# Performance work log

Measured on AMD Instinct MI355X. Metric: run time of the kernel, lower is better.

## Reference

```python
import jax, jax.numpy as jnp
import numpy as np

LOG2PI = float(np.log(2.0 * np.pi))


def _diag_gauss_logprob(x, mean, var):
    # clamp variance like torch's clamp_min(1e-10)
    var = jnp.maximum(var, 1e-10)
    return -0.5 * jnp.sum(jnp.log(var) + LOG2PI + (x - mean) ** 2 / var, axis=-1)


def setup_inputs() -> dict:
    key = jax.random.key(0)
    k1, k2, k3, k4, k5 = jax.random.split(key, 5)
    B, T, D = 256, 1024, 256
    y = jax.random.normal(k1, (B, T, D), dtype=jnp.float32)
    # strictly increasing time grid per dim (broadcast 2D form [T, D])
    dt = jax.random.uniform(k2, (T, D), dtype=jnp.float32, minval=1e-3, maxval=1e-2)
    ts_batch = jnp.cumsum(dt, axis=0)
    # learned params around their torch inits (mu=0.0, logk=logs=-0.7)
    mu = 0.0 + 0.05 * jax.random.normal(k3, (D,), dtype=jnp.float32)
    log_kappa = -0.7 + 0.05 * jax.random.normal(k4, (D,), dtype=jnp.float32)
    log_sigma = -0.7 + 0.05 * jax.random.normal(k5, (D,), dtype=jnp.float32)
    return {"y": y, "ts_batch": ts_batch, "mu": mu,
            "log_kappa": log_kappa, "log_sigma": log_sigma}


def reference(y, ts_batch, mu, log_kappa, log_sigma):
    # y: [B, T, D]; ts_batch: [T, D] (or [B, T, D]); params: [D]
    kappa = jax.nn.softplus(log_kappa) + 1e-6
    sigma = jax.nn.softplus(log_sigma) + 1e-6
    if ts_batch.ndim == 2:
        ts = ts_batch[None, :, :]  # broadcast over batch
    else:
        ts = ts_batch

    # stationary initial distribution: N(mu, sigma^2 / (2 kappa))
    var0 = sigma ** 2 / (2.0 * kappa)
    lp0 = _diag_gauss_logprob(y[:, 0, :], mu, var0)  # [B]

    # exact OU transition densities for all steps at once
    dt = jnp.maximum(ts[:, 1:, :] - ts[:, :-1, :], 1e-6)  # [*, T-1, D]
    Ad = jnp.exp(-kappa * dt)
    mean = mu + Ad * (y[:, :-1, :] - mu)                  # [B, T-1, D]
    q = sigma ** 2 * (1.0 - jnp.exp(-2.0 * kappa * dt)) / (2.0 * kappa)
    lp_trans = jnp.sum(_diag_gauss_logprob(y[:, 1:, :], mean, q), axis=1)  # [B]
    return lp0 + lp_trans
```

## Files before the change

kernel.cpp:

```cpp
#include <hip/hip_runtime.h>

#define LOG2PI 1.8378770664093453f

__global__ __launch_bounds__(256) void ou_lp_kernel(
    const float* __restrict__ y,
    const float* __restrict__ ts,
    const float* __restrict__ mu,
    const float* __restrict__ lk,
    const float* __restrict__ ls,
    float* __restrict__ out,
    int B, int T, int D)
{
    const int b    = blockIdx.y;
    const int widx = threadIdx.x >> 6;
    const int lane = threadIdx.x & 63;
    const int d4   = lane * 4;
    const int NW   = gridDim.x * 4;
    const int gw   = blockIdx.x * 4 + widx;
    const int NT   = T - 1;
    const int lo   = 1 + (NT * gw) / NW;
    const int hi   = 1 + (NT * (gw + 1)) / NW;

    const float4 muv = *(const float4*)(mu + d4);
    const float4 lkv = *(const float4*)(lk + d4);
    const float4 lsv = *(const float4*)(ls + d4);

    float mur[4]   = {muv.x, muv.y, muv.z, muv.w};
    float lkr[4]   = {lkv.x, lkv.y, lkv.z, lkv.w};
    float lsr[4]   = {lsv.x, lsv.y, lsv.z, lsv.w};
    float kap[4], s2[4], inv2k[4];
    #pragma unroll
    for (int j = 0; j < 4; ++j) {
        float xk = lkr[j];
        float kappa = fmaxf(xk, 0.0f) + log1pf(__expf(-fabsf(xk)));
        kappa += 1e-6f;
        float xs = lsr[j];
        float sigma = fmaxf(xs, 0.0f) + log1pf(__expf(-fabsf(xs)));
        sigma += 1e-6f;
        kap[j]   = kappa;
        s2[j]    = sigma * sigma;
        inv2k[j] = 0.5f / kappa;
    }

    const size_t ybase = (size_t)b * T * D;
    float ypc[4], tsp[4], acc[4];
    {
        const float4 y0 = *(const float4*)(y  + ybase + (size_t)(lo - 1) * D + d4);
        const float4 t0 = *(const float4*)(ts + (size_t)(lo - 1) * D + d4);
        ypc[0] = y0.x - mur[0]; ypc[1] = y0.y - mur[1];
        ypc[2] = y0.z - mur[2]; ypc[3] = y0.w - mur[3];
        tsp[0] = t0.x; tsp[1] = t0.y; tsp[2] = t0.z; tsp[3] = t0.w;
    }
    acc[0] = acc[1] = acc[2] = acc[3] = 0.0f;

    if (gw == 0) {
        #pragma unroll
        for (int j = 0; j < 4; ++j) {
            float var0 = fmaxf(s2[j] * inv2k[j], 1e-10f);
            float yc   = ypc[j];
            acc[j] += __logf(var0) + LOG2PI + __fdividef(yc * yc, var0);
        }
    }

    for (int t = lo; t < hi; ++t) {
        const float4 yt = *(const float4*)(y  + ybase + (size_t)t * D + d4);
        const float4 tt = *(const float4*)(ts + (size_t)t * D + d4);
        float ytr[4] = {yt.x, yt.y, yt.z, yt.w};
        float ttr[4] = {tt.x, tt.y, tt.z, tt.w};
        #pragma unroll
        for (int j = 0; j < 4; ++j) {
            float dt = fmaxf(ttr[j] - tsp[j], 1e-6f);
            float e  = __expf(-kap[j] * dt);
            float q  = fmaxf(s2[j] * (1.0f - e * e) * inv2k[j], 1e-10f);
            float yc = ytr[j] - mur[j];
            float r  = yc - e * ypc[j];
            acc[j] += __logf(q) + LOG2PI + __fdividef(r * r, q);
            ypc[j] = yc;
            tsp[j] = ttr[j];
        }
    }

    float s = (acc[0] + acc[1]) + (acc[2] + acc[3]);
    #pragma unroll
    for (int off = 32; off > 0; off >>= 1)
        s += __shfl_down(s, off);

    __shared__ float wsum[4];
    if (lane == 0) wsum[widx] = s;
    __syncthreads();
    if (threadIdx.x == 0) {
        float tot = (wsum[0] + wsum[1]) + (wsum[2] + wsum[3]);
        atomicAdd(out + b, -0.5f * tot);
    }
}

extern "C" void kernel_launch(void* const* d_in, const int* in_sizes, int n_in,
                              void* d_out, int out_size, void* d_ws, size_t ws_size,
                              hipStream_t stream) {
    const float* y  = (const float*)d_in[0];
    const float* ts = (const float*)d_in[1];
    const float* mu = (const float*)d_in[2];
    const float* lk = (const float*)d_in[3];
    const float* ls = (const float*)d_in[4];
    float* out = (float*)d_out;

    const int D = in_sizes[2];
    const int T = in_sizes[1] / D;
    const int B = in_sizes[0] / (T * D);

    hipMemsetAsync(d_out, 0, (size_t)out_size * sizeof(float), stream);

    dim3 grid(4, B);
    dim3 block(256);
    ou_lp_kernel<<<grid, block, 0, stream>>>(y, ts, mu, lk, ls, out, B, T, D);
}
```

Measured before the change: 400.4 us.

## Precompute batch-invariant OU transition terms once, then run a streaming quadratic-form kernel

Adds a precompute kernel that evaluates the time-grid and parameter terms once over [T, D], since none of them depend on the batch. It stores the decay factor and the inverse transition variance to workspace and sums the log-variance constants into one scalar. The main kernel then only streams y with a few FMAs per element, instead of doing an exp, a log and a divide per element in every batch. It also doubles the grid width, adds a one-step register prefetch, and adds a second launch, an extra memset and an atomic accumulation of the constant.

```diff
diff --git a/kernel.cpp b/kernel.cpp
--- a/kernel.cpp
+++ b/kernel.cpp
@@ -2,12 +2,66 @@
 
 #define LOG2PI 1.8378770664093453f
 
-__global__ __launch_bounds__(256) void ou_lp_kernel(
+
+__device__ __forceinline__ float block_reduce_add(float v, float* lds) {
+    #pragma unroll
+    for (int off = 32; off > 0; off >>= 1)
+        v += __shfl_down(v, off);
+    const int widx = threadIdx.x >> 6;
+    const int lane = threadIdx.x & 63;
+    if (lane == 0) lds[widx] = v;
+    __syncthreads();
+    float tot = 0.0f;
+    if (threadIdx.x == 0) {
+        const int nw = blockDim.x >> 6;
+        for (int i = 0; i < nw; ++i) tot += lds[i];
+    }
+    return tot;
+}
+
+__global__ void ou_precompute_kernel(
+    const float* __restrict__ ts, const float* __restrict__ lk,
+    const float* __restrict__ ls,
+    float* __restrict__ C, float* __restrict__ invvar0,
+    float* __restrict__ Ad, float* __restrict__ invq,
+    int T, int D)
+{
+    const int t = blockIdx.x;
+    const int d = threadIdx.x;
+
+    float xk = lk[d];
+    float kappa = fmaxf(xk, 0.0f) + log1pf(expf(-fabsf(xk))) + 1e-6f;
+    float xs = ls[d];
+    float sg = fmaxf(xs, 0.0f) + log1pf(expf(-fabsf(xs))) + 1e-6f;
+    float s2 = sg * sg;
+    float inv2k = 0.5f / kappa;
+
+    float val;
+    if (t == 0) {
+        float var0 = fmaxf(s2 * inv2k, 1e-10f);
+        invvar0[d] = 1.0f / var0;
+        val = logf(var0) + LOG2PI;
+    } else {
+        float dt = fmaxf(ts[t * D + d] - ts[(t - 1) * D + d], 1e-6f);
+        float e  = expf(-kappa * dt);
+        float q  = fmaxf(s2 * (1.0f - e * e) * inv2k, 1e-10f);
+        Ad[t * D + d]   = e;
+        invq[t * D + d] = 1.0f / q;
+        val = logf(q) + LOG2PI;
+    }
+
+    __shared__ float lds[8];
+    float tot = block_reduce_add(val, lds);
+    if (threadIdx.x == 0) atomicAdd(C, tot);
+}
+
+__global__ __launch_bounds__(256, 8) void ou_quad_kernel(
     const float* __restrict__ y,
-    const float* __restrict__ ts,
     const float* __restrict__ mu,
-    const float* __restrict__ lk,
-    const float* __restrict__ ls,
+    const float* __restrict__ C,
+    const float* __restrict__ invvar0,
+    const float* __restrict__ Ad,
+    const float* __restrict__ invq,
     float* __restrict__ out,
     int B, int T, int D)
 {
@@ -22,62 +76,51 @@
     const int hi   = 1 + (NT * (gw + 1)) / NW;
 
     const float4 muv = *(const float4*)(mu + d4);
-    const float4 lkv = *(const float4*)(lk + d4);
-    const float4 lsv = *(const float4*)(ls + d4);
-
-    float mur[4]   = {muv.x, muv.y, muv.z, muv.w};
-    float lkr[4]   = {lkv.x, lkv.y, lkv.z, lkv.w};
-    float lsr[4]   = {lsv.x, lsv.y, lsv.z, lsv.w};
-    float kap[4], s2[4], inv2k[4];
-    #pragma unroll
-    for (int j = 0; j < 4; ++j) {
-        float xk = lkr[j];
-        float kappa = fmaxf(xk, 0.0f) + log1pf(__expf(-fabsf(xk)));
-        kappa += 1e-6f;
-        float xs = lsr[j];
-        float sigma = fmaxf(xs, 0.0f) + log1pf(__expf(-fabsf(xs)));
-        sigma += 1e-6f;
-        kap[j]   = kappa;
-        s2[j]    = sigma * sigma;
-        inv2k[j] = 0.5f / kappa;
-    }
+    float mur[4] = {muv.x, muv.y, muv.z, muv.w};
 
     const size_t ybase = (size_t)b * T * D;
-    float ypc[4], tsp[4], acc[4];
+    float ypc[4], acc[4];
     {
-        const float4 y0 = *(const float4*)(y  + ybase + (size_t)(lo - 1) * D + d4);
-        const float4 t0 = *(const float4*)(ts + (size_t)(lo - 1) * D + d4);
+        const float4 y0 = *(const float4*)(y + ybase + (size_t)(lo - 1) * D + d4);
         ypc[0] = y0.x - mur[0]; ypc[1] = y0.y - mur[1];
         ypc[2] = y0.z - mur[2]; ypc[3] = y0.w - mur[3];
-        tsp[0] = t0.x; tsp[1] = t0.y; tsp[2] = t0.z; tsp[3] = t0.w;
     }
     acc[0] = acc[1] = acc[2] = acc[3] = 0.0f;
 
     if (gw == 0) {
+        const float4 iv = *(const float4*)(invvar0 + d4);
+        float ivr[4] = {iv.x, iv.y, iv.z, iv.w};
+        #pragma unroll
+        for (int j = 0; j < 4; ++j) acc[j] += ypc[j] * ypc[j] * ivr[j];
+    }
+
+    const float* yp = y   + ybase + (size_t)lo * D + d4;
+    const float* ap = Ad  + (size_t)lo * D + d4;
+    const float* qp = invq + (size_t)lo * D + d4;
+
+    float4 ycur = *(const float4*)yp;
+    float4 acur = *(const float4*)ap;
+    float4 qcur = *(const float4*)qp;
+    for (int t = lo; t < hi; ++t) {
+        float4 ynxt, anxt, qnxt;
+        if (t + 1 < hi) {
+            ynxt = *(const float4*)(yp + D);
+            anxt = *(const float4*)(ap + D);
+            qnxt = *(const float4*)(qp + D);
+        }
+        yp += D; ap += D; qp += D;
+
+        float ytr[4] = {ycur.x, ycur.y, ycur.z, ycur.w};
+        float adr[4] = {acur.x, acur.y, acur.z, acur.w};
+        float iqr[4] = {qcur.x, qcur.y, qcur.z, qcur.w};
         #pragma unroll
         for (int j = 0; j < 4; ++j) {
-            float var0 = fmaxf(s2[j] * inv2k[j], 1e-10f);
-            float yc   = ypc[j];
-            acc[j] += __logf(var0) + LOG2PI + __fdividef(yc * yc, var0);
+            float yc = ytr[j] - mur[j];
+            float r  = fmaf(-adr[j], ypc[j], yc);
+            acc[j]   = fmaf(r * r, iqr[j], acc[j]);
+            ypc[j]   = yc;
         }
-    }
-
-    for (int t = lo; t < hi; ++t) {
-        const float4 yt = *(const float4*)(y  + ybase + (size_t)t * D + d4);
-        const float4 tt = *(const float4*)(ts + (size_t)t * D + d4);
-        float ytr[4] = {yt.x, yt.y, yt.z, yt.w};
-        float ttr[4] = {tt.x, tt.y, tt.z, tt.w};
-        #pragma unroll
-        for (int j = 0; j < 4; ++j) {
-            float dt = fmaxf(ttr[j] - tsp[j], 1e-6f);
-            float e  = __expf(-kap[j] * dt);
-            float q  = fmaxf(s2[j] * (1.0f - e * e) * inv2k[j], 1e-10f);
-            float yc = ytr[j] - mur[j];
-            float r  = yc - e * ypc[j];
-            acc[j] += __logf(q) + LOG2PI + __fdividef(r * r, q);
-            ypc[j] = yc;
-            tsp[j] = ttr[j];
-        }
+        ycur = ynxt; acur = anxt; qcur = qnxt;
     }
 
     float s = (acc[0] + acc[1]) + (acc[2] + acc[3]);
@@ -90,6 +133,7 @@
     __syncthreads();
     if (threadIdx.x == 0) {
         float tot = (wsum[0] + wsum[1]) + (wsum[2] + wsum[3]);
+        if (blockIdx.x == 0) tot += C[0];
         atomicAdd(out + b, -0.5f * tot);
     }
 }
@@ -108,9 +152,19 @@
     const int T = in_sizes[1] / D;
     const int B = in_sizes[0] / (T * D);
 
+    char* ws = (char*)d_ws;
+    float* C       = (float*)(ws);
+    float* invvar0 = (float*)(ws + 256);
+    float* Ad      = (float*)(ws + 4096);
+    float* invq    = (float*)(ws + 4096 + (size_t)T * D * sizeof(float));
+
     hipMemsetAsync(d_out, 0, (size_t)out_size * sizeof(float), stream);
+    hipMemsetAsync(C, 0, sizeof(float), stream);
 
-    dim3 grid(4, B);
-    dim3 block(256);
-    ou_lp_kernel<<<grid, block, 0, stream>>>(y, ts, mu, lk, ls, out, B, T, D);
+    ou_precompute_kernel<<<dim3(T), dim3(D), 0, stream>>>(
+        ts, lk, ls, C, invvar0, Ad, invq, T, D);
+
+    dim3 grid(8, B);
+    ou_quad_kernel<<<grid, dim3(256), 0, stream>>>(
+        y, mu, C, invvar0, Ad, invq, out, B, T, D);
 }
```

Measured after the change: 386.8 us. 3.4% less time.

## Process two batches per thread to share time-dependent transcendentals and prefetch loads

Applied to the files above, without the earlier changes.

Each thread now handles two batch rows at once, so the exp, log and reciprocal of the per-step variance, which depend only on time and dimension, are computed once and reused for both rows. The next step's y and ts loads are software-prefetched, y is read with nontemporal loads, and the grid changes to 8 column splits over B/2 row pairs with a launch-bounds occupancy hint. This halves transcendental work and ts reads per byte of y, which matters because the kernel streams about 268 MB of y. In exchange it adds register pressure and assumes B is even.

```diff
diff --git a/kernel.cpp b/kernel.cpp
--- a/kernel.cpp
+++ b/kernel.cpp
@@ -2,7 +2,9 @@
 
 #define LOG2PI 1.8378770664093453f
 
-__global__ __launch_bounds__(256) void ou_lp_kernel(
+typedef float f4 __attribute__((ext_vector_type(4)));
+
+__global__ __launch_bounds__(256, 4) void ou_fused_kernel(
     const float* __restrict__ y,
     const float* __restrict__ ts,
     const float* __restrict__ mu,
@@ -11,7 +13,8 @@
     float* __restrict__ out,
     int B, int T, int D)
 {
-    const int b    = blockIdx.y;
+    const int b0   = blockIdx.y * 2;
+    const int b1   = b0 + 1;
     const int widx = threadIdx.x >> 6;
     const int lane = threadIdx.x & 63;
     const int d4   = lane * 4;
@@ -21,76 +24,109 @@
     const int lo   = 1 + (NT * gw) / NW;
     const int hi   = 1 + (NT * (gw + 1)) / NW;
 
-    const float4 muv = *(const float4*)(mu + d4);
-    const float4 lkv = *(const float4*)(lk + d4);
-    const float4 lsv = *(const float4*)(ls + d4);
-
-    float mur[4]   = {muv.x, muv.y, muv.z, muv.w};
-    float lkr[4]   = {lkv.x, lkv.y, lkv.z, lkv.w};
-    float lsr[4]   = {lsv.x, lsv.y, lsv.z, lsv.w};
-    float kap[4], s2[4], inv2k[4];
+    const f4 muv = *(const f4*)(mu + d4);
+    const f4 lkv = *(const f4*)(lk + d4);
+    const f4 lsv = *(const f4*)(ls + d4);
+    float mur[4], kap[4], sv[4];
     #pragma unroll
     for (int j = 0; j < 4; ++j) {
-        float xk = lkr[j];
-        float kappa = fmaxf(xk, 0.0f) + log1pf(__expf(-fabsf(xk)));
-        kappa += 1e-6f;
-        float xs = lsr[j];
-        float sigma = fmaxf(xs, 0.0f) + log1pf(__expf(-fabsf(xs)));
-        sigma += 1e-6f;
-        kap[j]   = kappa;
-        s2[j]    = sigma * sigma;
-        inv2k[j] = 0.5f / kappa;
+        mur[j] = muv[j];
+        float xk = lkv[j];
+        float kappa = fmaxf(xk, 0.0f) + log1pf(__expf(-fabsf(xk))) + 1e-6f;
+        float xs = lsv[j];
+        float sg = fmaxf(xs, 0.0f) + log1pf(__expf(-fabsf(xs))) + 1e-6f;
+        kap[j] = kappa;
+        sv[j]  = (sg * sg) * (0.5f / kappa);
     }
 
-    const size_t ybase = (size_t)b * T * D;
-    float ypc[4], tsp[4], acc[4];
+    const size_t yb0 = (size_t)b0 * T * D;
+    const size_t yb1 = (size_t)b1 * T * D;
+    float tsp[4], yc0[4], yc1[4];
     {
-        const float4 y0 = *(const float4*)(y  + ybase + (size_t)(lo - 1) * D + d4);
-        const float4 t0 = *(const float4*)(ts + (size_t)(lo - 1) * D + d4);
-        ypc[0] = y0.x - mur[0]; ypc[1] = y0.y - mur[1];
-        ypc[2] = y0.z - mur[2]; ypc[3] = y0.w - mur[3];
-        tsp[0] = t0.x; tsp[1] = t0.y; tsp[2] = t0.z; tsp[3] = t0.w;
+        const f4 t0 = *(const f4*)(ts + (size_t)(lo - 1) * D + d4);
+        const f4 a0 = __builtin_nontemporal_load((const f4*)(y + yb0 + (size_t)(lo - 1) * D + d4));
+        const f4 a1 = __builtin_nontemporal_load((const f4*)(y + yb1 + (size_t)(lo - 1) * D + d4));
+        #pragma unroll
+        for (int j = 0; j < 4; ++j) {
+            tsp[j] = t0[j];
+            yc0[j] = a0[j] - mur[j];
+            yc1[j] = a1[j] - mur[j];
+        }
     }
-    acc[0] = acc[1] = acc[2] = acc[3] = 0.0f;
+
+    float aq0[4] = {0,0,0,0};
+    float aq1[4] = {0,0,0,0};
+    float al[4]  = {0,0,0,0};
 
     if (gw == 0) {
         #pragma unroll
         for (int j = 0; j < 4; ++j) {
-            float var0 = fmaxf(s2[j] * inv2k[j], 1e-10f);
-            float yc   = ypc[j];
-            acc[j] += __logf(var0) + LOG2PI + __fdividef(yc * yc, var0);
+            float var0 = fmaxf(sv[j], 1e-10f);
+            float iv   = __fdividef(1.0f, var0);
+            al[j]  += __logf(var0) + LOG2PI;
+            aq0[j] += yc0[j] * yc0[j] * iv;
+            aq1[j] += yc1[j] * yc1[j] * iv;
         }
     }
 
+    const float* tp  = ts + (size_t)lo * D + d4;
+    const float* y0p = y + yb0 + (size_t)lo * D + d4;
+    const float* y1p = y + yb1 + (size_t)lo * D + d4;
+
+    f4 tc = *(const f4*)tp;
+    f4 c0 = __builtin_nontemporal_load((const f4*)y0p);
+    f4 c1 = __builtin_nontemporal_load((const f4*)y1p);
+
     for (int t = lo; t < hi; ++t) {
-        const float4 yt = *(const float4*)(y  + ybase + (size_t)t * D + d4);
-        const float4 tt = *(const float4*)(ts + (size_t)t * D + d4);
-        float ytr[4] = {yt.x, yt.y, yt.z, yt.w};
-        float ttr[4] = {tt.x, tt.y, tt.z, tt.w};
+        f4 tn, n0, n1;
+        if (t + 1 < hi) {
+            tn = *(const f4*)(tp + D);
+            n0 = __builtin_nontemporal_load((const f4*)(y0p + D));
+            n1 = __builtin_nontemporal_load((const f4*)(y1p + D));
+        }
+        tp += D; y0p += D; y1p += D;
+
         #pragma unroll
         for (int j = 0; j < 4; ++j) {
-            float dt = fmaxf(ttr[j] - tsp[j], 1e-6f);
+            float dt = fmaxf(tc[j] - tsp[j], 1e-6f);
+            tsp[j]   = tc[j];
             float e  = __expf(-kap[j] * dt);
-            float q  = fmaxf(s2[j] * (1.0f - e * e) * inv2k[j], 1e-10f);
-            float yc = ytr[j] - mur[j];
-            float r  = yc - e * ypc[j];
-            acc[j] += __logf(q) + LOG2PI + __fdividef(r * r, q);
-            ypc[j] = yc;
-            tsp[j] = ttr[j];
+            float q  = fmaxf(sv[j] * (1.0f - e * e), 1e-10f);
+            float iq = __fdividef(1.0f, q);
+            al[j]   += __logf(q) + LOG2PI;
+
+            float a = c0[j] - mur[j];
+            float r = fmaf(-e, yc0[j], a);
+            aq0[j]  = fmaf(r * r, iq, aq0[j]);
+            yc0[j]  = a;
+
+            float bb = c1[j] - mur[j];
+            float r1 = fmaf(-e, yc1[j], bb);
+            aq1[j]   = fmaf(r1 * r1, iq, aq1[j]);
+            yc1[j]   = bb;
         }
+        tc = tn; c0 = n0; c1 = n1;
     }
 
-    float s = (acc[0] + acc[1]) + (acc[2] + acc[3]);
+    float s0 = (aq0[0] + aq0[1]) + (aq0[2] + aq0[3]);
+    float s1 = (aq1[0] + aq1[1]) + (aq1[2] + aq1[3]);
+    float sl = (al[0]  + al[1])  + (al[2]  + al[3]);
     #pragma unroll
-    for (int off = 32; off > 0; off >>= 1)
-        s += __shfl_down(s, off);
+    for (int off = 32; off > 0; off >>= 1) {
+        s0 += __shfl_down(s0, off);
+        s1 += __shfl_down(s1, off);
+        sl += __shfl_down(sl, off);
+    }
 
-    __shared__ float wsum[4];
-    if (lane == 0) wsum[widx] = s;
+    __shared__ float w0[4], w1[4], wl[4];
+    if (lane == 0) { w0[widx] = s0; w1[widx] = s1; wl[widx] = sl; }
     __syncthreads();
     if (threadIdx.x == 0) {
-        float tot = (wsum[0] + wsum[1]) + (wsum[2] + wsum[3]);
-        atomicAdd(out + b, -0.5f * tot);
+        float A0 = (w0[0] + w0[1]) + (w0[2] + w0[3]);
+        float A1 = (w1[0] + w1[1]) + (w1[2] + w1[3]);
+        float AL = (wl[0] + wl[1]) + (wl[2] + wl[3]);
+        atomicAdd(out + b0, -0.5f * (A0 + AL));
+        atomicAdd(out + b1, -0.5f * (A1 + AL));
     }
 }
 
@@ -110,7 +146,6 @@
 
     hipMemsetAsync(d_out, 0, (size_t)out_size * sizeof(float), stream);
 
-    dim3 grid(4, B);
-    dim3 block(256);
-    ou_lp_kernel<<<grid, block, 0, stream>>>(y, ts, mu, lk, ls, out, B, T, D);
+    dim3 grid(8, B / 2);
+    ou_fused_kernel<<<grid, dim3(256), 0, stream>>>(y, ts, mu, lk, ls, out, B, T, D);
 }
```

New measurement: 348.5 us. -13.0%, faster.
